# Optimization experiments

Measured on AMD Instinct MI355X. Metric: run time of the kernel, lower is better.

Reference implementation:

```python
import jax, jax.numpy as jnp
import numpy as np

PRUNE_RATIO = 0.5
NOISE_SCALE = 0.1
MIXUP_ALPHA = 0.05
TEMPERATURE = 0.5
B, N, D = 32, 4096, 256


def setup_inputs() -> dict:
    key = jax.random.key(0)
    k1, k2, k3 = jax.random.split(key, 3)
    seq = jax.random.normal(k1, (B, N, D), dtype=jnp.float32)
    attn_weights = jax.random.uniform(k2, (B, N), dtype=jnp.float32)
    uniform_noise = jax.random.uniform(k3, (B, N), dtype=jnp.float32)
    return {"seq": seq, "attn_weights": attn_weights, "uniform_noise": uniform_noise}


def reference(seq, attn_weights, uniform_noise):
    b, n, d = seq.shape
    k = max(1, int(n * (1.0 - PRUNE_RATIO)))
    # training branch: gumbel noise from the provided uniform draw
    gumbel = -jnp.log(-jnp.log(uniform_noise + 1e-10) + 1e-10)
    noisy = attn_weights + NOISE_SCALE * gumbel                      # (B, N)
    soft = jax.nn.softmax(noisy / TEMPERATURE, axis=-1)              # (B, N)
    _, top_idx = jax.lax.top_k(soft, k)                              # (B, K) int32
    # gather selected tokens: (B, K, D)
    selected = jnp.take_along_axis(seq, top_idx[:, :, None], axis=1)
    # mixup: mean of the pruned (non-selected) tokens
    mask = jnp.ones((b, n), dtype=seq.dtype).at[
        jnp.arange(b)[:, None], top_idx
    ].set(0.0)                                                       # (B, N), 1 on pruned
    remaining_sum = jnp.einsum('bn,bnd->bd', mask, seq)              # (B, D)
    remaining_count = mask.sum(axis=1, keepdims=True) + 1e-10        # (B, 1)
    remaining_mean = remaining_sum / remaining_count                 # (B, D)
    return selected + MIXUP_ALPHA * remaining_mean[:, None, :]       # (B, K, D)
```

## Files before the change

kernel.cpp:

```cpp
#include <hip/hip_runtime.h>

#define B_ 32
#define N_ 4096
#define D_ 256
#define K_ 2048

__global__ __launch_bounds__(256) void key_kernel(
    const float* __restrict__ attn, const float* __restrict__ noise,
    unsigned long long* __restrict__ keys, float* __restrict__ meanAccum) {
  const int t = blockIdx.x * 256 + threadIdx.x;
  float u = noise[t];
  float a = attn[t];
  float x = __fadd_rn(u, 1e-10f);
  float l1 = (float)log((double)x);
  float inner = __fadd_rn(-l1, 1e-10f);
  float g = -(float)log((double)inner);
  float noisy = __fadd_rn(a, __fmul_rn(0.1f, g));
  unsigned int fb = __float_as_uint(noisy);
  fb = (fb & 0x80000000u) ? ~fb : (fb | 0x80000000u);
  int i = t & (N_ - 1);
  keys[t] = ((unsigned long long)fb << 32) | (unsigned int)(~i);
  if (t < B_ * D_) meanAccum[t] = 0.0f;
}

__global__ __launch_bounds__(256) void rank_mean_kernel(
    const unsigned long long* __restrict__ keys, const float* __restrict__ seq,
    int* __restrict__ sortedIdx, float* __restrict__ meanAccum) {
  const int b = blockIdx.y;
  const int i = blockIdx.x * 256 + threadIdx.x;
  const unsigned long long* __restrict__ bk = keys + (size_t)b * N_;
  const unsigned long long ki = bk[i];

  int rank = 0;
  const ulonglong4* __restrict__ bk4 = (const ulonglong4*)bk;
#pragma unroll 4
  for (int j = 0; j < N_ / 4; ++j) {
    ulonglong4 v = bk4[j];
    rank += (v.x > ki);
    rank += (v.y > ki);
    rank += (v.z > ki);
    rank += (v.w > ki);
  }
  sortedIdx[(size_t)b * N_ + rank] = i;

  __shared__ int plist[256];
  __shared__ int pcount;
  if (threadIdx.x == 0) pcount = 0;
  __syncthreads();
  if (rank >= K_) {
    int slot = atomicAdd(&pcount, 1);
    plist[slot] = i;
  }
  __syncthreads();
  const int cnt = pcount;

  const int dv = threadIdx.x & 63;
  const int sub = threadIdx.x >> 6;
  float4 acc = make_float4(0.f, 0.f, 0.f, 0.f);
  for (int r = sub; r < cnt; r += 4) {
    const float4* row = (const float4*)(seq + ((size_t)b * N_ + plist[r]) * D_);
    float4 v = row[dv];
    acc.x += v.x; acc.y += v.y; acc.z += v.z; acc.w += v.w;
  }

  __shared__ float4 red[4][64];
  red[sub][dv] = acc;
  __syncthreads();
  if (sub == 0) {
    float4 s0 = red[0][dv], s1 = red[1][dv], s2 = red[2][dv], s3 = red[3][dv];
    float sx = s0.x + s1.x + s2.x + s3.x;
    float sy = s0.y + s1.y + s2.y + s3.y;
    float sz = s0.z + s1.z + s2.z + s3.z;
    float sw = s0.w + s1.w + s2.w + s3.w;
    float* dst = meanAccum + b * D_ + dv * 4;
    atomicAdd(dst + 0, sx);
    atomicAdd(dst + 1, sy);
    atomicAdd(dst + 2, sz);
    atomicAdd(dst + 3, sw);
  }
}

__global__ __launch_bounds__(256) void out_kernel(
    const float* __restrict__ seq, const int* __restrict__ sortedIdx,
    const float* __restrict__ meanAccum, float* __restrict__ out) {
  const unsigned int t = blockIdx.x * 256u + threadIdx.x;
  const int dv = t & 63;
  const int j = (t >> 6) & (K_ - 1);
  const int b = t >> 17;

  int idx = sortedIdx[b * N_ + j];
  float4 v = ((const float4*)(seq + ((size_t)b * N_ + idx) * D_))[dv];
  float4 m = ((const float4*)(meanAccum + b * D_))[dv];
  const float inv_cnt = 1.0f / 2048.0f;
  float4 o;
  o.x = v.x + 0.05f * (m.x * inv_cnt);
  o.y = v.y + 0.05f * (m.y * inv_cnt);
  o.z = v.z + 0.05f * (m.z * inv_cnt);
  o.w = v.w + 0.05f * (m.w * inv_cnt);
  ((float4*)out)[t] = o;
}

extern "C" void kernel_launch(void* const* d_in, const int* in_sizes, int n_in,
                              void* d_out, int out_size, void* d_ws, size_t ws_size,
                              hipStream_t stream) {
  const float* seq  = (const float*)d_in[0];
  const float* attn = (const float*)d_in[1];
  const float* nois = (const float*)d_in[2];
  float* out = (float*)d_out;

  int* sortedIdx   = (int*)d_ws;
  float* meanAccum = (float*)((char*)d_ws + (size_t)B_ * N_ * 4);
  unsigned long long* keys =
      (unsigned long long*)((char*)d_ws + (size_t)B_ * N_ * 4 + (size_t)B_ * D_ * 4);

  key_kernel<<<(B_ * N_) / 256, 256, 0, stream>>>(attn, nois, keys, meanAccum);
  rank_mean_kernel<<<dim3(N_ / 256, B_), 256, 0, stream>>>(keys, seq, sortedIdx, meanAccum);
  const int total4 = B_ * K_ * (D_ / 4);
  out_kernel<<<total4 / 256, 256, 0, stream>>>(seq, sortedIdx, meanAccum, out);
}
```

Measured before the change: 313.6 us.

## Split rank counting into tiled LDS kernel with per-thread multi-element ranks

Rank counting moves out of the combined rank/mean kernel into a separate kernel. Each block stages a 512-key slice in shared memory, each thread ranks eight keys against it, and partial counts are merged with atomics into a rank buffer. This replaces the old pattern where every thread streamed all 4096 keys from global memory, and it reuses each loaded key across eight comparisons. The cost is an extra kernel launch, a zeroed rank buffer and global atomics. With a 16x32 grid of 256-thread blocks, occupancy may also be limited.

```diff
diff --git a/kernel.cpp b/kernel.cpp
--- a/kernel.cpp
+++ b/kernel.cpp
@@ -5,9 +5,15 @@
 #define D_ 256
 #define K_ 2048
 
+#define ISPLIT 2
+#define JSPLIT 8
+#define EPT 8
+#define JSLICE (N_ / JSPLIT)
+
 __global__ __launch_bounds__(256) void key_kernel(
     const float* __restrict__ attn, const float* __restrict__ noise,
-    unsigned long long* __restrict__ keys, float* __restrict__ meanAccum) {
+    unsigned long long* __restrict__ keys, unsigned int* __restrict__ rankBuf,
+    float* __restrict__ meanAccum) {
   const int t = blockIdx.x * 256 + threadIdx.x;
   float u = noise[t];
   float a = attn[t];
@@ -20,27 +26,50 @@
   fb = (fb & 0x80000000u) ? ~fb : (fb | 0x80000000u);
   int i = t & (N_ - 1);
   keys[t] = ((unsigned long long)fb << 32) | (unsigned int)(~i);
+  rankBuf[t] = 0u;
   if (t < B_ * D_) meanAccum[t] = 0.0f;
 }
 
-__global__ __launch_bounds__(256) void rank_mean_kernel(
-    const unsigned long long* __restrict__ keys, const float* __restrict__ seq,
+__global__ __launch_bounds__(256) void rank_kernel(
+    const unsigned long long* __restrict__ keys,
+    unsigned int* __restrict__ rankBuf) {
+  const int b = blockIdx.y;
+  const int ic = blockIdx.x >> 3;
+  const int jc = blockIdx.x & (JSPLIT - 1);
+  __shared__ __align__(16) ulonglong2 lk2[JSLICE / 2];
+
+  const unsigned long long* __restrict__ bk = keys + (size_t)b * N_;
+
+  const ulonglong2* __restrict__ gk2 = (const ulonglong2*)(bk + jc * JSLICE);
+  lk2[threadIdx.x] = gk2[threadIdx.x];
+
+  const int ibase = ic * (N_ / ISPLIT) + threadIdx.x;
+  unsigned long long ki[EPT];
+#pragma unroll
+  for (int e = 0; e < EPT; ++e) ki[e] = bk[ibase + e * 256];
+  __syncthreads();
+
+  unsigned int rk[EPT] = {0u, 0u, 0u, 0u, 0u, 0u, 0u, 0u};
+#pragma unroll 4
+  for (int j = 0; j < JSLICE / 2; ++j) {
+    ulonglong2 v = lk2[j];
+#pragma unroll
+    for (int e = 0; e < EPT; ++e) {
+      rk[e] += (v.x > ki[e]);
+      rk[e] += (v.y > ki[e]);
+    }
+  }
+#pragma unroll
+  for (int e = 0; e < EPT; ++e)
+    atomicAdd(&rankBuf[(size_t)b * N_ + ibase + e * 256], rk[e]);
+}
+
+__global__ __launch_bounds__(256) void scatter_mean_kernel(
+    const unsigned int* __restrict__ rankBuf, const float* __restrict__ seq,
     int* __restrict__ sortedIdx, float* __restrict__ meanAccum) {
   const int b = blockIdx.y;
   const int i = blockIdx.x * 256 + threadIdx.x;
-  const unsigned long long* __restrict__ bk = keys + (size_t)b * N_;
-  const unsigned long long ki = bk[i];
-
-  int rank = 0;
-  const ulonglong4* __restrict__ bk4 = (const ulonglong4*)bk;
-#pragma unroll 4
-  for (int j = 0; j < N_ / 4; ++j) {
-    ulonglong4 v = bk4[j];
-    rank += (v.x > ki);
-    rank += (v.y > ki);
-    rank += (v.z > ki);
-    rank += (v.w > ki);
-  }
+  const unsigned int rank = rankBuf[(size_t)b * N_ + i];
   sortedIdx[(size_t)b * N_ + rank] = i;
 
   __shared__ int plist[256];
@@ -112,9 +141,12 @@
   float* meanAccum = (float*)((char*)d_ws + (size_t)B_ * N_ * 4);
   unsigned long long* keys =
       (unsigned long long*)((char*)d_ws + (size_t)B_ * N_ * 4 + (size_t)B_ * D_ * 4);
+  unsigned int* rankBuf =
+      (unsigned int*)((char*)keys + (size_t)B_ * N_ * 8);
 
-  key_kernel<<<(B_ * N_) / 256, 256, 0, stream>>>(attn, nois, keys, meanAccum);
-  rank_mean_kernel<<<dim3(N_ / 256, B_), 256, 0, stream>>>(keys, seq, sortedIdx, meanAccum);
+  key_kernel<<<(B_ * N_) / 256, 256, 0, stream>>>(attn, nois, keys, rankBuf, meanAccum);
+  rank_kernel<<<dim3(ISPLIT * JSPLIT, B_), 256, 0, stream>>>(keys, rankBuf);
+  scatter_mean_kernel<<<dim3(N_ / 256, B_), 256, 0, stream>>>(rankBuf, seq, sortedIdx, meanAccum);
   const int total4 = B_ * K_ * (D_ / 4);
   out_kernel<<<total4 / 256, 256, 0, stream>>>(seq, sortedIdx, meanAccum, out);
 }
```

New measurement: 262.8 us. 16.2% less time.
